# Performance work log

Measured on AMD Instinct MI355X. Metric: run time of the kernel, lower is better.

## Reference

```python
import jax, jax.numpy as jnp
import numpy as np

N, E, B = 50000, 800000, 64
H, D, FIN = 2, 128, 128  # heads, per-head dim, input feat dim
L = 2  # lstm layers


def segment_softmax(logits, seg, num_segments):
    # logits: [E, ...] softmax over entries sharing seg id (leading axis)
    m = jax.ops.segment_max(logits, seg, num_segments=num_segments)
    e = jnp.exp(logits - m[seg])
    s = jax.ops.segment_sum(e, seg, num_segments=num_segments)
    return e / s[seg]


def gat_layer(x, W, al, ar, b, src, dst):
    # DGL GATConv: fc -> per-edge LeakyReLU score -> edge softmax over dst -> aggregate
    h = (x @ W).reshape(N, H, D)                      # [N,H,D]
    el = jnp.sum(h * al, axis=-1)                     # [N,H]
    er = jnp.sum(h * ar, axis=-1)                     # [N,H]
    e = jax.nn.leaky_relu(el[src] + er[dst], 0.2)     # [E,H]
    alpha = segment_softmax(e, dst, N)                # [E,H]
    out = jax.ops.segment_sum(alpha[:, :, None] * h[src], dst, num_segments=N)
    return out + b                                    # [N,H,D]


def global_attention_pool(x, wg, bg, seg):
    gate = x @ wg + bg                                # [N,1]
    alpha = segment_softmax(gate, seg, B)             # [N,1]
    return jax.ops.segment_sum(alpha * x, seg, num_segments=B)  # [B,F]


def lstm(xs, Wih, Whh, bih, bhh):
    # xs: [T,B,Hd]; params stacked over layers [L,4Hd,Hd]/[L,4Hd]; torch gate order i,f,g,o
    Hd = Whh.shape[-1]
    h = None
    for l in range(Wih.shape[0]):
        def step(carry, x_t, l=l):
            h, c = carry
            gates = x_t @ Wih[l].T + h @ Whh[l].T + bih[l] + bhh[l]
            i, f, g, o = jnp.split(gates, 4, axis=-1)
            c = jax.nn.sigmoid(f) * c + jax.nn.sigmoid(i) * jnp.tanh(g)
            h = jax.nn.sigmoid(o) * jnp.tanh(c)
            return (h, c), h
        init = (jnp.zeros((xs.shape[1], Hd), xs.dtype), jnp.zeros((xs.shape[1], Hd), xs.dtype))
        (h, _), xs = jax.lax.scan(step, init, xs)
    return h  # final hidden state of last layer [B,Hd]


def setup_inputs() -> dict:
    key = jax.random.key(0)
    ks = jax.random.split(key, 32)
    s = 0.1
    inp = {
        "nfeats": jax.random.normal(ks[0], (N, FIN), jnp.float32),
        "src": jax.random.randint(ks[1], (E,), 0, N, jnp.int32),
        "dst": jax.random.randint(ks[2], (E,), 0, N, jnp.int32),
        "node_graph": jnp.sort(jax.random.randint(ks[3], (N,), 0, B, jnp.int32)),
    }
    for i, ink in enumerate([(FIN, ks[4], ks[5], ks[6], ks[7]), (D, ks[8], ks[9], ks[10], ks[11]), (D, ks[12], ks[13], ks[14], ks[15])]):
        fin, kw, kl, kr, kb = ink
        inp[f"W{i+1}"] = jax.random.normal(kw, (fin, H * D), jnp.float32) * s
        inp[f"al{i+1}"] = jax.random.normal(kl, (H, D), jnp.float32) * s
        inp[f"ar{i+1}"] = jax.random.normal(kr, (H, D), jnp.float32) * s
        inp[f"b{i+1}"] = jnp.zeros((H, D), jnp.float32)
    for i in range(4):
        inp[f"gw{i}"] = jax.random.normal(ks[16 + i], (D, 1), jnp.float32) * s
        inp[f"gb{i}"] = jnp.zeros((1,), jnp.float32)
    inp["Wih"] = jax.random.normal(ks[20], (L, 4 * D, D), jnp.float32) * s
    inp["Whh"] = jax.random.normal(ks[21], (L, 4 * D, D), jnp.float32) * s
    inp["bih"] = jnp.zeros((L, 4 * D), jnp.float32)
    inp["bhh"] = jnp.zeros((L, 4 * D), jnp.float32)
    inp["cw"] = jax.random.normal(ks[22], (D, 1), jnp.float32) * s
    inp["cb"] = jnp.zeros((1,), jnp.float32)
    return inp


def reference(nfeats, src, dst, node_graph,
              W1, al1, ar1, b1, W2, al2, ar2, b2, W3, al3, ar3, b3,
              gw0, gb0, gw1, gb1, gw2, gb2, gw3, gb3,
              Wih, Whh, bih, bhh, cw, cb):
    hg0 = global_attention_pool(nfeats, gw0, gb0, node_graph)
    h = jnp.mean(jax.nn.relu(gat_layer(nfeats, W1, al1, ar1, b1, src, dst)), axis=1)
    hg1 = global_attention_pool(h, gw1, gb1, node_graph)
    h = jnp.mean(jax.nn.relu(gat_layer(h, W2, al2, ar2, b2, src, dst)), axis=1)
    hg2 = global_attention_pool(h, gw2, gb2, node_graph)
    h = jnp.mean(jax.nn.relu(gat_layer(h, W3, al3, ar3, b3, src, dst)), axis=1)
    hg3 = global_attention_pool(h, gw3, gb3, node_graph)
    seq = jnp.stack((hg0, hg1, hg2, hg3), axis=0)     # [4,B,D]
    last_h = lstm(seq, Wih, Whh, bih, bhh)            # [B,D] (dropout: eval mode, identity)
    return jax.nn.sigmoid(last_h @ cw + cb)           # [B,1]
```

## Files before the change

### kernel.cpp

```cpp
#include <hip/hip_runtime.h>
#include <cmath>


typedef __attribute__((ext_vector_type(8))) short short8v;
typedef __attribute__((ext_vector_type(4))) float float4v;
typedef __attribute__((ext_vector_type(2))) float float2v;

__device__ __forceinline__ float sigmoidf_(float x){ return 1.f/(1.f+expf(-x)); }
__device__ __forceinline__ float fexp(float x){ return __expf(x); }

__device__ __forceinline__ unsigned f2bf_rne(float f){
  unsigned u = __float_as_uint(f);
  return (u + 0x7fffu + ((u >> 16) & 1u)) >> 16;
}
__device__ __forceinline__ float bf2f(ushort v){ return __uint_as_float((unsigned)v << 16); }
__device__ __forceinline__ unsigned char f2fp8(float f){
  unsigned v = __builtin_amdgcn_cvt_pk_fp8_f32(f, f, 0, false);
  return (unsigned char)(v & 0xffu);
}

__global__ void k_hist(const int* __restrict__ dst, int* __restrict__ deg, int E){
  int e = blockIdx.x*blockDim.x + threadIdx.x;
  if (e < E) atomicAdd(&deg[dst[e]], 1);
}

#define CHUNK 1024
__global__ __launch_bounds__(256) void k_chunksum(const int* __restrict__ in, int* __restrict__ csum, int n){
  int b = blockIdx.x;
  int tid = threadIdx.x;
  int v = 0;
  #pragma unroll
  for (int k = 0; k < 4; k++){
    int i = b*CHUNK + tid + k*256;
    if (i < n) v += in[i];
  }
  for (int d = 1; d < 64; d <<= 1) v += __shfl_xor(v, d);
  __shared__ int ws[4];
  if ((tid & 63) == 0) ws[tid>>6] = v;
  __syncthreads();
  if (tid == 0) csum[b] = ws[0]+ws[1]+ws[2]+ws[3];
}

__global__ void k_scan_small(const int* __restrict__ csum, int* __restrict__ cpre, int nb,
                             int* __restrict__ total_out){
  int lane = threadIdx.x;
  int v = (lane < nb) ? csum[lane] : 0;
  int incl = v;
  for (int d = 1; d < 64; d <<= 1){ int t = __shfl_up(incl, d); if (lane >= d) incl += t; }
  if (lane < nb) cpre[lane] = incl - v;
  if (lane == 63) *total_out = incl;
}

__global__ __launch_bounds__(256) void k_scan_apply(const int* __restrict__ in, const int* __restrict__ cpre,
                                                    int* __restrict__ offs, int n){
  int b = blockIdx.x;
  int tid = threadIdx.x, lane = tid & 63, wid = tid >> 6;
  int x[4];
  int s = 0;
  #pragma unroll
  for (int k = 0; k < 4; k++){
    int i = b*CHUNK + tid*4 + k;
    x[k] = (i < n) ? in[i] : 0;
    s += x[k];
  }
  int incl = s;
  for (int d = 1; d < 64; d <<= 1){ int t = __shfl_up(incl, d); if (lane >= d) incl += t; }
  __shared__ int ws[4];
  if (lane == 63) ws[wid] = incl;
  __syncthreads();
  int wpre = 0;
  for (int w = 0; w < wid; w++) wpre += ws[w];
  int base = cpre[b] + wpre + incl - s;
  #pragma unroll
  for (int k = 0; k < 4; k++){
    int i = b*CHUNK + tid*4 + k;
    if (i < n) offs[i] = base;
    base += x[k];
  }
}

__global__ void k_scatter_src(const int* __restrict__ src, const int* __restrict__ dst,
                              const int* __restrict__ offs, int* __restrict__ cnt,
                              int* __restrict__ srcP, int E){
  int e = blockIdx.x*blockDim.x + threadIdx.x;
  if (e < E){ int d = dst[e]; int p = atomicAdd(&cnt[d], 1); srcP[offs[d] + p] = src[e]; }
}

__global__ void k_graph_bounds(const int* __restrict__ ng, int* __restrict__ gstart, int n, int nb){
  int i = blockIdx.x*blockDim.x + threadIdx.x;
  if (i >= n) return;
  int g = ng[i];
  int gp = (i == 0) ? -1 : ng[i-1];
  for (int b = gp+1; b <= g; b++) gstart[b] = i;
  if (i == n-1) for (int b = g+1; b <= nb; b++) gstart[b] = n;
}

__global__ __launch_bounds__(256) void k_tobf16_gate(const float* __restrict__ in,
    const float* __restrict__ gw, const float* __restrict__ gb,
    ushort* __restrict__ out, float* __restrict__ gate, int Nn){
  int n = blockIdx.x*4 + (threadIdx.x >> 6);
  if (n >= Nn) return;
  int lane = threadIdx.x & 63;
  float2 v = *(const float2*)(in + (size_t)n*128 + lane*2);
  unsigned pk = (f2bf_rne(v.y) << 16) | f2bf_rne(v.x);
  *(unsigned*)(out + (size_t)n*128 + lane*2) = pk;
  float2 gv = *(const float2*)(gw + lane*2);
  float p = v.x*gv.x + v.y*gv.y;
  for (int k = 1; k < 64; k <<= 1) p += __shfl_xor(p, k);
  if (lane == 0) gate[n] = p + gb[0];
}

__global__ void k_wt(const float* __restrict__ W, ushort* __restrict__ Wt, int total){
  int idx = blockIdx.x*blockDim.x + threadIdx.x;
  if (idx >= total) return;
  int c = idx >> 7;
  int k = idx & 127;
  Wt[idx] = (ushort)f2bf_rne(W[(size_t)k*256 + c]);
}

__global__ void k_lstm_prep(const float* __restrict__ Wih, const float* __restrict__ Whh,
                            const float* __restrict__ bih, const float* __restrict__ bhh,
                            unsigned* __restrict__ Wxp, unsigned* __restrict__ Whp,
                            float* __restrict__ bias2){
  int idx = blockIdx.x*blockDim.x + threadIdx.x;
  if (idx >= 131072) return;
  int j   = idx & 511;
  int c   = (idx >> 9) & 63;
  int isH = (idx >> 15) & 1;
  int l   = idx >> 16;
  const float* srcW = isH ? Whh : Wih;
  float w0 = srcW[(size_t)l*512*128 + (size_t)j*128 + 2*c];
  float w1 = srcW[(size_t)l*512*128 + (size_t)j*128 + 2*c + 1];
  unsigned v = (f2bf_rne(w1) << 16) | f2bf_rne(w0);
  unsigned* dst = isH ? Whp : Wxp;
  dst[(size_t)l*32768 + c*512 + j] = v;
  if (!isH && c == 0) bias2[l*512 + j] = bih[l*512 + j] + bhh[l*512 + j];
}

__global__ __launch_bounds__(256) void k_gemm_mfma(const ushort* __restrict__ Xh,
    const ushort* __restrict__ Wt, const float* __restrict__ alv, const float* __restrict__ arv,
    unsigned char* __restrict__ Y8, float* __restrict__ el, float* __restrict__ er, int M){
  __shared__ ushort WlS[16*256*8];
  int tid = threadIdx.x;
  #pragma unroll
  for (int i = 0; i < 16; i++){
    int g = i*256 + tid;
    int row = g >> 4, c = g & 15;
    *(uint4*)(WlS + ((size_t)c*256 + row)*8) = *(const uint4*)(Wt + (size_t)row*128 + c*8);
  }
  __syncthreads();
  int wave = tid >> 6;
  int lane = tid & 63;
  int strip = blockIdx.x*4 + wave;
  if (strip*16 >= M) return;
  int m0 = strip*16;
  int l15 = lane & 15;
  int kg  = lane >> 4;
  int arow = m0 + l15; if (arow >= M) arow = M-1;
  short8v a[4];
  const ushort* xrow = Xh + (size_t)arow*128 + kg*8;
  #pragma unroll
  for (int ks = 0; ks < 4; ks++) a[ks] = *(const short8v*)(xrow + ks*32);
  float4v acc[16];
  #pragma unroll
  for (int nt = 0; nt < 16; nt++) acc[nt] = (float4v){0.f,0.f,0.f,0.f};
  #pragma unroll
  for (int nt = 0; nt < 16; nt++){
    #pragma unroll
    for (int ks = 0; ks < 4; ks++){
      short8v b = *(const short8v*)(WlS + (((size_t)(kg + ks*4)*256) + nt*16 + l15)*8);
      acc[nt] = __builtin_amdgcn_mfma_f32_16x16x32_bf16(a[ks], b, acc[nt], 0, 0, 0);
    }
  }
  float pel0[4]={0,0,0,0}, pel1[4]={0,0,0,0}, per0[4]={0,0,0,0}, per1[4]={0,0,0,0};
  #pragma unroll
  for (int nt = 0; nt < 16; nt++){
    int col = nt*16 + l15;
    float av = alv[col], rv = arv[col];
    #pragma unroll
    for (int j = 0; j < 4; j++){
      float v = acc[nt][j];
      int r = m0 + kg*4 + j;
      if (r < M) Y8[(size_t)r*256 + col] = f2fp8(v);
      if (nt < 8){ pel0[j] += v*av; per0[j] += v*rv; }
      else       { pel1[j] += v*av; per1[j] += v*rv; }
    }
  }
  #pragma unroll
  for (int j = 0; j < 4; j++){
    #pragma unroll
    for (int d = 1; d < 16; d <<= 1){
      pel0[j] += __shfl_xor(pel0[j], d);
      pel1[j] += __shfl_xor(pel1[j], d);
      per0[j] += __shfl_xor(per0[j], d);
      per1[j] += __shfl_xor(per1[j], d);
    }
  }
  if (l15 == 0){
    #pragma unroll
    for (int j = 0; j < 4; j++){
      int r = m0 + kg*4 + j;
      if (r < M){
        el[(size_t)r*2+0] = pel0[j];
        el[(size_t)r*2+1] = pel1[j];
        er[(size_t)r*2+0] = per0[j];
        er[(size_t)r*2+1] = per1[j];
      }
    }
  }
}

#define MAXE 256
__global__ __launch_bounds__(256) void k_aggregate(const unsigned char* __restrict__ hpair8,
    const float* __restrict__ el, const float* __restrict__ er,
    const int* __restrict__ srcP, const int* __restrict__ offs,
    const float* __restrict__ bias, const float* __restrict__ gwv, const float* __restrict__ gbv,
    ushort* __restrict__ outh, float* __restrict__ gate, int Nn){
  __shared__ float sw[4][MAXE][2];
  __shared__ int   ss[4][MAXE];
  int wave = threadIdx.x >> 6;
  int n = blockIdx.x*4 + wave;
  if (n >= Nn) return;
  int lane = threadIdx.x & 63;
  int e0 = offs[n], e1 = offs[n+1];
  int deg = e1 - e0;
  int quarter = lane >> 4;
  int sub     = lane & 15;
  int head    = sub >> 3;
  float2 erv = *(const float2*)(er + (size_t)n*2);
  float2v acc[8];
  #pragma unroll
  for (int k = 0; k < 8; k++) acc[k] = (float2v){0.f, 0.f};
  float inv0, inv1;

  if (deg <= MAXE){
    float m0 = -3.4e38f, m1 = -3.4e38f;
    for (int i = lane; i < deg; i += 64){
      int s = srcP[e0 + i];
      ss[wave][i] = s;
      float2 lv = *(const float2*)(el + (size_t)s*2);
      float v0 = lv.x + erv.x, v1 = lv.y + erv.y;
      v0 = (v0 > 0.f) ? v0 : 0.2f*v0;
      v1 = (v1 > 0.f) ? v1 : 0.2f*v1;
      sw[wave][i][0] = v0; sw[wave][i][1] = v1;
      m0 = fmaxf(m0, v0); m1 = fmaxf(m1, v1);
    }
    for (int k = 1; k < 64; k <<= 1){ m0 = fmaxf(m0, __shfl_xor(m0, k)); m1 = fmaxf(m1, __shfl_xor(m1, k)); }
    float s0 = 0.f, s1 = 0.f;
    for (int i = lane; i < deg; i += 64){
      float x0 = fexp(sw[wave][i][0] - m0);
      float x1 = fexp(sw[wave][i][1] - m1);
      sw[wave][i][0] = x0; sw[wave][i][1] = x1;
      s0 += x0; s1 += x1;
    }
    for (int k = 1; k < 64; k <<= 1){ s0 += __shfl_xor(s0, k); s1 += __shfl_xor(s1, k); }
    inv0 = (s0 > 0.f) ? 1.f/s0 : 0.f;
    inv1 = (s1 > 0.f) ? 1.f/s1 : 0.f;
    for (int i = quarter; i < deg; i += 4){
      int s = ss[wave][i];
      float w = sw[wave][i][head];
      uint4 hv = *(const uint4*)(hpair8 + (size_t)s*256 + sub*16);
      float2v wv = { w, w };
      acc[0] += wv*__builtin_amdgcn_cvt_pk_f32_fp8(hv.x, false);
      acc[1] += wv*__builtin_amdgcn_cvt_pk_f32_fp8(hv.x, true);
      acc[2] += wv*__builtin_amdgcn_cvt_pk_f32_fp8(hv.y, false);
      acc[3] += wv*__builtin_amdgcn_cvt_pk_f32_fp8(hv.y, true);
      acc[4] += wv*__builtin_amdgcn_cvt_pk_f32_fp8(hv.z, false);
      acc[5] += wv*__builtin_amdgcn_cvt_pk_f32_fp8(hv.z, true);
      acc[6] += wv*__builtin_amdgcn_cvt_pk_f32_fp8(hv.w, false);
      acc[7] += wv*__builtin_amdgcn_cvt_pk_f32_fp8(hv.w, true);
    }
  } else {
    float m0 = -3.4e38f, m1 = -3.4e38f;
    for (int i = e0 + lane; i < e1; i += 64){
      int s = srcP[i];
      float2 lv = *(const float2*)(el + (size_t)s*2);
      float v0 = lv.x + erv.x, v1 = lv.y + erv.y;
      v0 = (v0 > 0.f) ? v0 : 0.2f*v0;
      v1 = (v1 > 0.f) ? v1 : 0.2f*v1;
      m0 = fmaxf(m0, v0); m1 = fmaxf(m1, v1);
    }
    for (int k = 1; k < 64; k <<= 1){ m0 = fmaxf(m0, __shfl_xor(m0, k)); m1 = fmaxf(m1, __shfl_xor(m1, k)); }
    float s0 = 0.f, s1 = 0.f;
    for (int i = e0 + lane; i < e1; i += 64){
      int s = srcP[i];
      float2 lv = *(const float2*)(el + (size_t)s*2);
      float v0 = lv.x + erv.x, v1 = lv.y + erv.y;
      v0 = (v0 > 0.f) ? v0 : 0.2f*v0;
      v1 = (v1 > 0.f) ? v1 : 0.2f*v1;
      s0 += fexp(v0 - m0); s1 += fexp(v1 - m1);
    }
    for (int k = 1; k < 64; k <<= 1){ s0 += __shfl_xor(s0, k); s1 += __shfl_xor(s1, k); }
    inv0 = (s0 > 0.f) ? 1.f/s0 : 0.f;
    inv1 = (s1 > 0.f) ? 1.f/s1 : 0.f;
    for (int c0 = e0; c0 < e1; c0 += 64){
      int ce = e1 - c0; if (ce > 64) ce = 64;
      if (lane < ce){
        int s = srcP[c0 + lane];
        float2 lv = *(const float2*)(el + (size_t)s*2);
        float v0 = lv.x + erv.x, v1 = lv.y + erv.y;
        v0 = (v0 > 0.f) ? v0 : 0.2f*v0;
        v1 = (v1 > 0.f) ? v1 : 0.2f*v1;
        ss[wave][lane] = s;
        sw[wave][lane][0] = fexp(v0 - m0);
        sw[wave][lane][1] = fexp(v1 - m1);
      }
      for (int i = quarter; i < ce; i += 4){
        int s = ss[wave][i];
        float w = sw[wave][i][head];
        uint4 hv = *(const uint4*)(hpair8 + (size_t)s*256 + sub*16);
        float2v wv = { w, w };
        acc[0] += wv*__builtin_amdgcn_cvt_pk_f32_fp8(hv.x, false);
        acc[1] += wv*__builtin_amdgcn_cvt_pk_f32_fp8(hv.x, true);
        acc[2] += wv*__builtin_amdgcn_cvt_pk_f32_fp8(hv.y, false);
        acc[3] += wv*__builtin_amdgcn_cvt_pk_f32_fp8(hv.y, true);
        acc[4] += wv*__builtin_amdgcn_cvt_pk_f32_fp8(hv.z, false);
        acc[5] += wv*__builtin_amdgcn_cvt_pk_f32_fp8(hv.z, true);
        acc[6] += wv*__builtin_amdgcn_cvt_pk_f32_fp8(hv.w, false);
        acc[7] += wv*__builtin_amdgcn_cvt_pk_f32_fp8(hv.w, true);
      }
    }
  }

  float inv = head ? inv1 : inv0;
  #pragma unroll
  for (int k = 0; k < 8; k++){
    float2v t16, t32;
    t16[0] = __shfl_xor(acc[k][0], 16); t16[1] = __shfl_xor(acc[k][1], 16);
    acc[k] += t16;
    t32[0] = __shfl_xor(acc[k][0], 32); t32[1] = __shfl_xor(acc[k][1], 32);
    acc[k] += t32;
  }
  float t[16];
  #pragma unroll
  for (int k = 0; k < 16; k++)
    t[k] = fmaxf(acc[k>>1][k&1]*inv + bias[sub*16 + k], 0.f);
  float o[16];
  #pragma unroll
  for (int k = 0; k < 16; k++) o[k] = 0.5f*(t[k] + __shfl_xor(t[k], 8));
  if (lane < 8){
    ushort u[16];
    #pragma unroll
    for (int k = 0; k < 16; k++) u[k] = (ushort)f2bf_rne(o[k]);
    *(uint4*)(outh + (size_t)n*128 + sub*16)     = *(uint4*)u;
    *(uint4*)(outh + (size_t)n*128 + sub*16 + 8) = *(uint4*)(u + 8);
    float gp = 0.f;
    #pragma unroll
    for (int k = 0; k < 16; k++) gp += o[k]*gwv[sub*16 + k];
    #pragma unroll
    for (int d = 1; d < 8; d <<= 1) gp += __shfl_xor(gp, d);
    if (sub == 0) gate[n] = gp + gbv[0];
  }
}

#define POOL_P 32
__global__ __launch_bounds__(128) void k_pool_partial(const ushort* __restrict__ x,
    const float* __restrict__ gate, const int* __restrict__ gstart,
    float* __restrict__ partials){
  int b = blockIdx.x;
  int p = blockIdx.y;
  int n0 = gstart[b], n1 = gstart[b+1];
  int tid = threadIdx.x, lane = tid & 63, wid = tid >> 6;
  __shared__ float red[2];
  float m = -3.4e38f;
  for (int n = n0 + tid; n < n1; n += 128) m = fmaxf(m, gate[n]);
  for (int k = 1; k < 64; k <<= 1) m = fmaxf(m, __shfl_xor(m, k));
  if (lane == 0) red[wid] = m;
  __syncthreads();
  m = fmaxf(red[0], red[1]);
  __syncthreads();
  float s = 0.f;
  for (int n = n0 + tid; n < n1; n += 128) s += __expf(gate[n] - m);
  for (int k = 1; k < 64; k <<= 1) s += __shfl_xor(s, k);
  if (lane == 0) red[wid] = s;
  __syncthreads();
  s = red[0] + red[1];
  float inv = (s > 0.f) ? 1.f/s : 0.f;
  float acc = 0.f;
  for (int n = n0 + p; n < n1; n += POOL_P){
    float w = __expf(gate[n] - m) * inv;
    acc += w * bf2f(x[(size_t)n*128 + tid]);
  }
  partials[((size_t)b*POOL_P + p)*128 + tid] = acc;
}

__global__ __launch_bounds__(128) void k_pool_reduce(const float* __restrict__ partials,
    float* __restrict__ hg){
  int b = blockIdx.x;
  int tid = threadIdx.x;
  float s = 0.f;
  #pragma unroll
  for (int p = 0; p < POOL_P; p++) s += partials[((size_t)b*POOL_P + p)*128 + tid];
  hg[(size_t)b*128 + tid] = s;
}

__global__ __launch_bounds__(512) void k_lstm_all(const float* __restrict__ seq,
    const unsigned* __restrict__ Wxp, const unsigned* __restrict__ Whp,
    const float* __restrict__ bias2,
    const float* __restrict__ cw, const float* __restrict__ cb,
    float* __restrict__ out, int B){
  int b = blockIdx.x;
  int j = threadIdx.x;
  __shared__ float xs[4][128];
  __shared__ float gates[512];
  __shared__ float hcur[128], ccur[128];
  __shared__ float l0out[4][128];
  __shared__ float red[2];

  #pragma unroll
  for (int l = 0; l < 2; l++){
    const unsigned* Wx = Wxp + (size_t)l*32768;
    const unsigned* Wh = Whp + (size_t)l*32768;
    const float* bi = bias2 + l*512;
    { int t = j >> 7, k = j & 127;
      xs[t][k] = (l == 0) ? seq[(size_t)t*B*128 + (size_t)b*128 + k] : l0out[t][k];
      if (j < 128){ hcur[j] = 0.f; ccur[j] = 0.f; } }
    __syncthreads();
    float gx[4] = {0.f, 0.f, 0.f, 0.f};
    #pragma unroll 8
    for (int c = 0; c < 64; c++){
      unsigned w2 = Wx[c*512 + j];
      float wlo = __uint_as_float(w2 << 16);
      float whi = __uint_as_float(w2 & 0xffff0000u);
      #pragma unroll
      for (int t = 0; t < 4; t++)
        gx[t] += xs[t][2*c]*wlo + xs[t][2*c+1]*whi;
    }
    #pragma unroll
    for (int t = 0; t < 4; t++){
      float g = gx[t] + bi[j];
      #pragma unroll 8
      for (int c = 0; c < 64; c++){
        unsigned w2 = Wh[c*512 + j];
        g += hcur[2*c]*__uint_as_float(w2 << 16)
           + hcur[2*c+1]*__uint_as_float(w2 & 0xffff0000u);
      }
      gates[j] = g;
      __syncthreads();
      if (j < 128){
        float gi = sigmoidf_(gates[j]);
        float gf = sigmoidf_(gates[128 + j]);
        float gg = tanhf(gates[256 + j]);
        float go = sigmoidf_(gates[384 + j]);
        float c2 = gf * ccur[j] + gi * gg;
        float h = go * tanhf(c2);
        ccur[j] = c2;
        hcur[j] = h;
        if (l == 0) l0out[t][j] = h;
      }
      __syncthreads();
    }
  }
  float p = (j < 128) ? hcur[j] * cw[j] : 0.f;
  if (j < 128){
    for (int k = 1; k < 64; k <<= 1) p += __shfl_xor(p, k);
    if ((j & 63) == 0) red[j >> 6] = p;
  }
  __syncthreads();
  if (j == 0) out[b] = sigmoidf_(red[0] + red[1] + cb[0]);
}

extern "C" void kernel_launch(void* const* d_in, const int* in_sizes, int n_in,
                              void* d_out, int out_size, void* d_ws, size_t ws_size,
                              hipStream_t stream){
  const float* nfeats = (const float*)d_in[0];
  const int*   src    = (const int*)d_in[1];
  const int*   dst    = (const int*)d_in[2];
  const int*   ng     = (const int*)d_in[3];
  const float* Wm[3]  = { (const float*)d_in[4],  (const float*)d_in[8],  (const float*)d_in[12] };
  const float* al[3]  = { (const float*)d_in[5],  (const float*)d_in[9],  (const float*)d_in[13] };
  const float* ar[3]  = { (const float*)d_in[6],  (const float*)d_in[10], (const float*)d_in[14] };
  const float* bb[3]  = { (const float*)d_in[7],  (const float*)d_in[11], (const float*)d_in[15] };
  const float* gw[4]  = { (const float*)d_in[16], (const float*)d_in[18], (const float*)d_in[20], (const float*)d_in[22] };
  const float* gb[4]  = { (const float*)d_in[17], (const float*)d_in[19], (const float*)d_in[21], (const float*)d_in[23] };
  const float* Wih = (const float*)d_in[24];
  const float* Whh = (const float*)d_in[25];
  const float* bih = (const float*)d_in[26];
  const float* bhh = (const float*)d_in[27];
  const float* cw  = (const float*)d_in[28];
  const float* cb  = (const float*)d_in[29];

  const int N = in_sizes[3];
  const int E = in_sizes[1];
  const int B = out_size;

  char* p = (char*)d_ws;
  auto alloc = [&](size_t bytes) -> void* {
    void* q = (void*)p;
    p += (bytes + 255) & ~(size_t)255;
    return q;
  };
  unsigned char* hpair8 = (unsigned char*)alloc((size_t)N*256);
  ushort* aggh   = (ushort*)alloc((size_t)N*128*2);
  ushort* xh0    = (ushort*)alloc((size_t)N*128*2);
  ushort* Wt     = (ushort*)alloc((size_t)3*256*128*2);
  float*  el     = (float*)alloc((size_t)N*2*4);
  float*  er     = (float*)alloc((size_t)N*2*4);
  int*    srcP   = (int*)alloc((size_t)E*4);
  float*  gate   = (float*)alloc((size_t)N*4);
  int*    deg    = (int*)alloc((size_t)N*4);
  int*    offs   = (int*)alloc((size_t)(N+1)*4);
  int*    cnt    = (int*)alloc((size_t)N*4);
  int*    gstart = (int*)alloc((size_t)(B+1)*4);
  int*    csum   = (int*)alloc((size_t)64*4);
  int*    cpre   = (int*)alloc((size_t)64*4);
  float*  seqA   = (float*)alloc((size_t)4*B*128*4);
  float*  partials = (float*)alloc((size_t)B*POOL_P*128*4);
  unsigned* Wxp  = (unsigned*)alloc((size_t)2*64*512*4);
  unsigned* Whp  = (unsigned*)alloc((size_t)2*64*512*4);
  float*  bias2  = (float*)alloc((size_t)2*512*4);

  auto cdiv = [](int a, int b){ return (a + b - 1) / b; };
  const int NB = cdiv(N, CHUNK);

  hipMemsetAsync(deg, 0, (size_t)N*4, stream);
  hipMemsetAsync(cnt, 0, (size_t)N*4, stream);
  k_hist<<<cdiv(E,256), 256, 0, stream>>>(dst, deg, E);
  k_chunksum<<<NB, 256, 0, stream>>>(deg, csum, N);
  k_scan_small<<<1, 64, 0, stream>>>(csum, cpre, NB, offs + N);
  k_scan_apply<<<NB, 256, 0, stream>>>(deg, cpre, offs, N);
  k_scatter_src<<<cdiv(E,256), 256, 0, stream>>>(src, dst, offs, cnt, srcP, E);
  k_graph_bounds<<<cdiv(N,256), 256, 0, stream>>>(ng, gstart, N, B);

  k_tobf16_gate<<<cdiv(N,4), 256, 0, stream>>>(nfeats, gw[0], gb[0], xh0, gate, N);
  for (int l = 0; l < 3; l++)
    k_wt<<<cdiv(256*128, 256), 256, 0, stream>>>(Wm[l], Wt + (size_t)l*256*128, 256*128);
  k_lstm_prep<<<cdiv(131072, 256), 256, 0, stream>>>(Wih, Whh, bih, bhh, Wxp, Whp, bias2);

  auto pool_rest = [&](const ushort* xv, float* hgv){
    dim3 pg(B, POOL_P);
    k_pool_partial<<<pg, 128, 0, stream>>>(xv, gate, gstart, partials);
    k_pool_reduce<<<B, 128, 0, stream>>>(partials, hgv);
  };

  pool_rest(xh0, seqA + 0*(size_t)B*128);

  const ushort* xh = xh0;
  const int strips = cdiv(N, 16);
  for (int layer = 0; layer < 3; layer++){
    k_gemm_mfma<<<cdiv(strips,4), 256, 0, stream>>>(xh, Wt + (size_t)layer*256*128,
        al[layer], ar[layer], hpair8, el, er, N);
    k_aggregate<<<cdiv(N,4), 256, 0, stream>>>(hpair8, el, er, srcP, offs,
        bb[layer], gw[layer+1], gb[layer+1], aggh, gate, N);
    pool_rest(aggh, seqA + (size_t)(layer+1)*B*128);
    xh = aggh;
  }

  k_lstm_all<<<B, 512, 0, stream>>>(seqA, Wxp, Whp, bias2, cw, cb, (float*)d_out, B);
}
```

Before: 422.8 us.

## Fuse prep kernels, co-schedule pooling with GEMM, fold scan and pool reduction

```diff
diff --git a/kernel.cpp b/kernel.cpp
--- a/kernel.cpp
+++ b/kernel.cpp
@@ -41,20 +41,19 @@
   if (tid == 0) csum[b] = ws[0]+ws[1]+ws[2]+ws[3];
 }
 
-__global__ void k_scan_small(const int* __restrict__ csum, int* __restrict__ cpre, int nb,
-                             int* __restrict__ total_out){
-  int lane = threadIdx.x;
-  int v = (lane < nb) ? csum[lane] : 0;
-  int incl = v;
-  for (int d = 1; d < 64; d <<= 1){ int t = __shfl_up(incl, d); if (lane >= d) incl += t; }
-  if (lane < nb) cpre[lane] = incl - v;
-  if (lane == 63) *total_out = incl;
-}
-
-__global__ __launch_bounds__(256) void k_scan_apply(const int* __restrict__ in, const int* __restrict__ cpre,
-                                                    int* __restrict__ offs, int n){
+__global__ __launch_bounds__(256) void k_scan_apply(const int* __restrict__ in, const int* __restrict__ csum,
+                                                    int* __restrict__ offs, int n, int nb){
   int b = blockIdx.x;
   int tid = threadIdx.x, lane = tid & 63, wid = tid >> 6;
+  __shared__ int s_cpre;
+  __shared__ int ws[4];
+  if (tid < 64){
+    int v = (tid < nb) ? csum[tid] : 0;
+    int icl = v;
+    for (int d = 1; d < 64; d <<= 1){ int t = __shfl_up(icl, d); if (lane >= d) icl += t; }
+    if (tid == b) s_cpre = icl - v;
+  }
+  __syncthreads();
   int x[4];
   int s = 0;
   #pragma unroll
@@ -65,18 +64,18 @@
   }
   int incl = s;
   for (int d = 1; d < 64; d <<= 1){ int t = __shfl_up(incl, d); if (lane >= d) incl += t; }
-  __shared__ int ws[4];
   if (lane == 63) ws[wid] = incl;
   __syncthreads();
   int wpre = 0;
   for (int w = 0; w < wid; w++) wpre += ws[w];
-  int base = cpre[b] + wpre + incl - s;
+  int base = s_cpre + wpre + incl - s;
   #pragma unroll
   for (int k = 0; k < 4; k++){
     int i = b*CHUNK + tid*4 + k;
     if (i < n) offs[i] = base;
     base += x[k];
   }
+  if (b == nb-1 && tid == 255) offs[n] = base;
 }
 
 __global__ void k_scatter_src(const int* __restrict__ src, const int* __restrict__ dst,
@@ -86,127 +85,176 @@
   if (e < E){ int d = dst[e]; int p = atomicAdd(&cnt[d], 1); srcP[offs[d] + p] = src[e]; }
 }
 
-__global__ void k_graph_bounds(const int* __restrict__ ng, int* __restrict__ gstart, int n, int nb){
-  int i = blockIdx.x*blockDim.x + threadIdx.x;
-  if (i >= n) return;
-  int g = ng[i];
-  int gp = (i == 0) ? -1 : ng[i-1];
-  for (int b = gp+1; b <= g; b++) gstart[b] = i;
-  if (i == n-1) for (int b = g+1; b <= nb; b++) gstart[b] = n;
-}
-
-__global__ __launch_bounds__(256) void k_tobf16_gate(const float* __restrict__ in,
-    const float* __restrict__ gw, const float* __restrict__ gb,
-    ushort* __restrict__ out, float* __restrict__ gate, int Nn){
-  int n = blockIdx.x*4 + (threadIdx.x >> 6);
-  if (n >= Nn) return;
-  int lane = threadIdx.x & 63;
-  float2 v = *(const float2*)(in + (size_t)n*128 + lane*2);
-  unsigned pk = (f2bf_rne(v.y) << 16) | f2bf_rne(v.x);
-  *(unsigned*)(out + (size_t)n*128 + lane*2) = pk;
-  float2 gv = *(const float2*)(gw + lane*2);
-  float p = v.x*gv.x + v.y*gv.y;
-  for (int k = 1; k < 64; k <<= 1) p += __shfl_xor(p, k);
-  if (lane == 0) gate[n] = p + gb[0];
-}
-
-__global__ void k_wt(const float* __restrict__ W, ushort* __restrict__ Wt, int total){
-  int idx = blockIdx.x*blockDim.x + threadIdx.x;
-  if (idx >= total) return;
-  int c = idx >> 7;
-  int k = idx & 127;
-  Wt[idx] = (ushort)f2bf_rne(W[(size_t)k*256 + c]);
-}
-
-__global__ void k_lstm_prep(const float* __restrict__ Wih, const float* __restrict__ Whh,
-                            const float* __restrict__ bih, const float* __restrict__ bhh,
-                            unsigned* __restrict__ Wxp, unsigned* __restrict__ Whp,
-                            float* __restrict__ bias2){
-  int idx = blockIdx.x*blockDim.x + threadIdx.x;
-  if (idx >= 131072) return;
-  int j   = idx & 511;
-  int c   = (idx >> 9) & 63;
-  int isH = (idx >> 15) & 1;
-  int l   = idx >> 16;
-  const float* srcW = isH ? Whh : Wih;
-  float w0 = srcW[(size_t)l*512*128 + (size_t)j*128 + 2*c];
-  float w1 = srcW[(size_t)l*512*128 + (size_t)j*128 + 2*c + 1];
-  unsigned v = (f2bf_rne(w1) << 16) | f2bf_rne(w0);
-  unsigned* dst = isH ? Whp : Wxp;
-  dst[(size_t)l*32768 + c*512 + j] = v;
-  if (!isH && c == 0) bias2[l*512 + j] = bih[l*512 + j] + bhh[l*512 + j];
-}
-
-__global__ __launch_bounds__(256) void k_gemm_mfma(const ushort* __restrict__ Xh,
+__global__ __launch_bounds__(256) void k_prep(
+    const int* __restrict__ ng, int* __restrict__ gstart,
+    const float* __restrict__ nfeats, const float* __restrict__ gw0, const float* __restrict__ gb0,
+    ushort* __restrict__ xh0, float* __restrict__ gate,
+    const float* __restrict__ W0, const float* __restrict__ W1, const float* __restrict__ W2,
+    ushort* __restrict__ Wt,
+    const float* __restrict__ Wih, const float* __restrict__ Whh,
+    const float* __restrict__ bih, const float* __restrict__ bhh,
+    unsigned* __restrict__ Wxp, unsigned* __restrict__ Whp, float* __restrict__ bias2,
+    int N, int B){
+  int tid = threadIdx.x;
+  int blk = blockIdx.x;
+  const int nbGB = (N + 255) >> 8;
+  const int nbTG = (N + 3) >> 2;
+  const int nbWT = (3*256*128) >> 8;
+  if (blk < nbGB){
+    int i = blk*256 + tid;
+    if (i >= N) return;
+    int g = ng[i];
+    int gp = (i == 0) ? -1 : ng[i-1];
+    for (int bb = gp+1; bb <= g; bb++) gstart[bb] = i;
+    if (i == N-1) for (int bb = g+1; bb <= B; bb++) gstart[bb] = N;
+    return;
+  }
+  blk -= nbGB;
+  if (blk < nbTG){
+    int n = blk*4 + (tid >> 6);
+    if (n >= N) return;
+    int lane = tid & 63;
+    float2 v = *(const float2*)(nfeats + (size_t)n*128 + lane*2);
+    unsigned pk = (f2bf_rne(v.y) << 16) | f2bf_rne(v.x);
+    *(unsigned*)(xh0 + (size_t)n*128 + lane*2) = pk;
+    float2 gv = *(const float2*)(gw0 + lane*2);
+    float p = v.x*gv.x + v.y*gv.y;
+    for (int k = 1; k < 64; k <<= 1) p += __shfl_xor(p, k);
+    if (lane == 0) gate[n] = p + gb0[0];
+    return;
+  }
+  blk -= nbTG;
+  if (blk < nbWT){
+    int idx = blk*256 + tid;
+    int layer = idx >> 15;
+    int within = idx & 32767;
+    int c = within >> 7;
+    int k = within & 127;
+    const float* W = (layer == 0) ? W0 : (layer == 1) ? W1 : W2;
+    Wt[idx] = (ushort)f2bf_rne(W[(size_t)k*256 + c]);
+    return;
+  }
+  blk -= nbWT;
+  {
+    int idx = blk*256 + tid;
+    if (idx >= 131072) return;
+    int j   = idx & 511;
+    int c   = (idx >> 9) & 63;
+    int isH = (idx >> 15) & 1;
+    int l   = idx >> 16;
+    const float* srcW = isH ? Whh : Wih;
+    float w0 = srcW[(size_t)l*512*128 + (size_t)j*128 + 2*c];
+    float w1 = srcW[(size_t)l*512*128 + (size_t)j*128 + 2*c + 1];
+    unsigned v = (f2bf_rne(w1) << 16) | f2bf_rne(w0);
+    unsigned* dstp = isH ? Whp : Wxp;
+    dstp[(size_t)l*32768 + c*512 + j] = v;
+    if (!isH && c == 0) bias2[l*512 + j] = bih[l*512 + j] + bhh[l*512 + j];
+  }
+}
+
+__global__ __launch_bounds__(256) void k_gemm_pool(const ushort* __restrict__ Xh,
     const ushort* __restrict__ Wt, const float* __restrict__ alv, const float* __restrict__ arv,
-    unsigned char* __restrict__ Y8, float* __restrict__ el, float* __restrict__ er, int M){
+    unsigned char* __restrict__ Y8, float* __restrict__ el, float* __restrict__ er, int M,
+    int gemmBlocks, const float* __restrict__ gate, const int* __restrict__ gstart,
+    float* __restrict__ partials){
   __shared__ ushort WlS[16*256*8];
   int tid = threadIdx.x;
-  #pragma unroll
-  for (int i = 0; i < 16; i++){
-    int g = i*256 + tid;
-    int row = g >> 4, c = g & 15;
-    *(uint4*)(WlS + ((size_t)c*256 + row)*8) = *(const uint4*)(Wt + (size_t)row*128 + c*8);
-  }
-  __syncthreads();
-  int wave = tid >> 6;
-  int lane = tid & 63;
-  int strip = blockIdx.x*4 + wave;
-  if (strip*16 >= M) return;
-  int m0 = strip*16;
-  int l15 = lane & 15;
-  int kg  = lane >> 4;
-  int arow = m0 + l15; if (arow >= M) arow = M-1;
-  short8v a[4];
-  const ushort* xrow = Xh + (size_t)arow*128 + kg*8;
-  #pragma unroll
-  for (int ks = 0; ks < 4; ks++) a[ks] = *(const short8v*)(xrow + ks*32);
-  float4v acc[16];
-  #pragma unroll
-  for (int nt = 0; nt < 16; nt++) acc[nt] = (float4v){0.f,0.f,0.f,0.f};
-  #pragma unroll
-  for (int nt = 0; nt < 16; nt++){
-    #pragma unroll
-    for (int ks = 0; ks < 4; ks++){
-      short8v b = *(const short8v*)(WlS + (((size_t)(kg + ks*4)*256) + nt*16 + l15)*8);
-      acc[nt] = __builtin_amdgcn_mfma_f32_16x16x32_bf16(a[ks], b, acc[nt], 0, 0, 0);
-    }
-  }
-  float pel0[4]={0,0,0,0}, pel1[4]={0,0,0,0}, per0[4]={0,0,0,0}, per1[4]={0,0,0,0};
-  #pragma unroll
-  for (int nt = 0; nt < 16; nt++){
-    int col = nt*16 + l15;
-    float av = alv[col], rv = arv[col];
+  if ((int)blockIdx.x < gemmBlocks){
+    #pragma unroll
+    for (int i = 0; i < 16; i++){
+      int g = i*256 + tid;
+      int row = g >> 4, c = g & 15;
+      *(uint4*)(WlS + ((size_t)c*256 + row)*8) = *(const uint4*)(Wt + (size_t)row*128 + c*8);
+    }
+    __syncthreads();
+    int wave = tid >> 6;
+    int lane = tid & 63;
+    int strip = blockIdx.x*4 + wave;
+    if (strip*16 >= M) return;
+    int m0 = strip*16;
+    int l15 = lane & 15;
+    int kg  = lane >> 4;
+    int arow = m0 + l15; if (arow >= M) arow = M-1;
+    short8v a[4];
+    const ushort* xrow = Xh + (size_t)arow*128 + kg*8;
+    #pragma unroll
+    for (int ks = 0; ks < 4; ks++) a[ks] = *(const short8v*)(xrow + ks*32);
+    float4v acc[16];
+    #pragma unroll
+    for (int nt = 0; nt < 16; nt++) acc[nt] = (float4v){0.f,0.f,0.f,0.f};
+    #pragma unroll
+    for (int nt = 0; nt < 16; nt++){
+      #pragma unroll
+      for (int ks = 0; ks < 4; ks++){
+        short8v b = *(const short8v*)(WlS + (((size_t)(kg + ks*4)*256) + nt*16 + l15)*8);
+        acc[nt] = __builtin_amdgcn_mfma_f32_16x16x32_bf16(a[ks], b, acc[nt], 0, 0, 0);
+      }
+    }
+    float pel0[4]={0,0,0,0}, pel1[4]={0,0,0,0}, per0[4]={0,0,0,0}, per1[4]={0,0,0,0};
+    #pragma unroll
+    for (int nt = 0; nt < 16; nt++){
+      int col = nt*16 + l15;
+      float av = alv[col], rv = arv[col];
+      #pragma unroll
+      for (int j = 0; j < 4; j++){
+        float v = acc[nt][j];
+        int r = m0 + kg*4 + j;
+        if (r < M) Y8[(size_t)r*256 + col] = f2fp8(v);
+        if (nt < 8){ pel0[j] += v*av; per0[j] += v*rv; }
+        else       { pel1[j] += v*av; per1[j] += v*rv; }
+      }
+    }
     #pragma unroll
     for (int j = 0; j < 4; j++){
-      float v = acc[nt][j];
-      int r = m0 + kg*4 + j;
-      if (r < M) Y8[(size_t)r*256 + col] = f2fp8(v);
-      if (nt < 8){ pel0[j] += v*av; per0[j] += v*rv; }
-      else       { pel1[j] += v*av; per1[j] += v*rv; }
-    }
-  }
-  #pragma unroll
-  for (int j = 0; j < 4; j++){
-    #pragma unroll
-    for (int d = 1; d < 16; d <<= 1){
-      pel0[j] += __shfl_xor(pel0[j], d);
-      pel1[j] += __shfl_xor(pel1[j], d);
-      per0[j] += __shfl_xor(per0[j], d);
-      per1[j] += __shfl_xor(per1[j], d);
-    }
-  }
-  if (l15 == 0){
-    #pragma unroll
-    for (int j = 0; j < 4; j++){
-      int r = m0 + kg*4 + j;
-      if (r < M){
-        el[(size_t)r*2+0] = pel0[j];
-        el[(size_t)r*2+1] = pel1[j];
-        er[(size_t)r*2+0] = per0[j];
-        er[(size_t)r*2+1] = per1[j];
-      }
-    }
+      #pragma unroll
+      for (int d = 1; d < 16; d <<= 1){
+        pel0[j] += __shfl_xor(pel0[j], d);
+        pel1[j] += __shfl_xor(pel1[j], d);
+        per0[j] += __shfl_xor(per0[j], d);
+        per1[j] += __shfl_xor(per1[j], d);
+      }
+    }
+    if (l15 == 0){
+      #pragma unroll
+      for (int j = 0; j < 4; j++){
+        int r = m0 + kg*4 + j;
+        if (r < M){
+          el[(size_t)r*2+0] = pel0[j];
+          el[(size_t)r*2+1] = pel1[j];
+          er[(size_t)r*2+0] = per0[j];
+          er[(size_t)r*2+1] = per1[j];
+        }
+      }
+    }
+  } else {
+    float* red = (float*)WlS;
+    int pb = blockIdx.x - gemmBlocks;
+    int b = pb >> 4;
+    int py = pb & 15;
+    int lane = tid & 63, wid = tid >> 6;
+    int n0 = gstart[b], n1 = gstart[b+1];
+    float m = -3.4e38f;
+    for (int n = n0 + tid; n < n1; n += 256) m = fmaxf(m, gate[n]);
+    for (int k = 1; k < 64; k <<= 1) m = fmaxf(m, __shfl_xor(m, k));
+    if (lane == 0) red[wid] = m;
+    __syncthreads();
+    m = fmaxf(fmaxf(red[0], red[1]), fmaxf(red[2], red[3]));
+    __syncthreads();
+    float s = 0.f;
+    for (int n = n0 + tid; n < n1; n += 256) s += __expf(gate[n] - m);
+    for (int k = 1; k < 64; k <<= 1) s += __shfl_xor(s, k);
+    if (lane == 0) red[wid] = s;
+    __syncthreads();
+    s = red[0] + red[1] + red[2] + red[3];
+    float inv = (s > 0.f) ? 1.f/s : 0.f;
+    int half = tid >> 7, t127 = tid & 127;
+    int p = py*2 + half;
+    float acc = 0.f;
+    for (int n = n0 + p; n < n1; n += 32){
+      float w = __expf(gate[n] - m) * inv;
+      acc += w * bf2f(Xh[(size_t)n*128 + t127]);
+    }
+    partials[((size_t)b*32 + p)*128 + t127] = acc;
   }
 }
 
@@ -353,48 +401,7 @@
   }
 }
 
-#define POOL_P 32
-__global__ __launch_bounds__(128) void k_pool_partial(const ushort* __restrict__ x,
-    const float* __restrict__ gate, const int* __restrict__ gstart,
-    float* __restrict__ partials){
-  int b = blockIdx.x;
-  int p = blockIdx.y;
-  int n0 = gstart[b], n1 = gstart[b+1];
-  int tid = threadIdx.x, lane = tid & 63, wid = tid >> 6;
-  __shared__ float red[2];
-  float m = -3.4e38f;
-  for (int n = n0 + tid; n < n1; n += 128) m = fmaxf(m, gate[n]);
-  for (int k = 1; k < 64; k <<= 1) m = fmaxf(m, __shfl_xor(m, k));
-  if (lane == 0) red[wid] = m;
-  __syncthreads();
-  m = fmaxf(red[0], red[1]);
-  __syncthreads();
-  float s = 0.f;
-  for (int n = n0 + tid; n < n1; n += 128) s += __expf(gate[n] - m);
-  for (int k = 1; k < 64; k <<= 1) s += __shfl_xor(s, k);
-  if (lane == 0) red[wid] = s;
-  __syncthreads();
-  s = red[0] + red[1];
-  float inv = (s > 0.f) ? 1.f/s : 0.f;
-  float acc = 0.f;
-  for (int n = n0 + p; n < n1; n += POOL_P){
-    float w = __expf(gate[n] - m) * inv;
-    acc += w * bf2f(x[(size_t)n*128 + tid]);
-  }
-  partials[((size_t)b*POOL_P + p)*128 + tid] = acc;
-}
-
-__global__ __launch_bounds__(128) void k_pool_reduce(const float* __restrict__ partials,
-    float* __restrict__ hg){
-  int b = blockIdx.x;
-  int tid = threadIdx.x;
-  float s = 0.f;
-  #pragma unroll
-  for (int p = 0; p < POOL_P; p++) s += partials[((size_t)b*POOL_P + p)*128 + tid];
-  hg[(size_t)b*128 + tid] = s;
-}
-
-__global__ __launch_bounds__(512) void k_lstm_all(const float* __restrict__ seq,
+__global__ __launch_bounds__(512) void k_lstm_all(const float* __restrict__ part4,
     const unsigned* __restrict__ Wxp, const unsigned* __restrict__ Whp,
     const float* __restrict__ bias2,
     const float* __restrict__ cw, const float* __restrict__ cb,
@@ -413,7 +420,15 @@
     const unsigned* Wh = Whp + (size_t)l*32768;
     const float* bi = bias2 + l*512;
     { int t = j >> 7, k = j & 127;
-      xs[t][k] = (l == 0) ? seq[(size_t)t*B*128 + (size_t)b*128 + k] : l0out[t][k];
+      if (l == 0){
+        const float* pp = part4 + (((size_t)t*B + b)*32)*128 + k;
+        float s = 0.f;
+        #pragma unroll
+        for (int p2 = 0; p2 < 32; p2++) s += pp[p2*128];
+        xs[t][k] = s;
+      } else {
+        xs[t][k] = l0out[t][k];
+      }
       if (j < 128){ hcur[j] = 0.f; ccur[j] = 0.f; } }
     __syncthreads();
     float gx[4] = {0.f, 0.f, 0.f, 0.f};
@@ -499,13 +514,11 @@
   int*    srcP   = (int*)alloc((size_t)E*4);
   float*  gate   = (float*)alloc((size_t)N*4);
   int*    deg    = (int*)alloc((size_t)N*4);
+  int*    cnt    = (int*)alloc((size_t)N*4);
   int*    offs   = (int*)alloc((size_t)(N+1)*4);
-  int*    cnt    = (int*)alloc((size_t)N*4);
   int*    gstart = (int*)alloc((size_t)(B+1)*4);
   int*    csum   = (int*)alloc((size_t)64*4);
-  int*    cpre   = (int*)alloc((size_t)64*4);
-  float*  seqA   = (float*)alloc((size_t)4*B*128*4);
-  float*  partials = (float*)alloc((size_t)B*POOL_P*128*4);
+  float*  part4  = (float*)alloc((size_t)4*B*32*128*4);
   unsigned* Wxp  = (unsigned*)alloc((size_t)2*64*512*4);
   unsigned* Whp  = (unsigned*)alloc((size_t)2*64*512*4);
   float*  bias2  = (float*)alloc((size_t)2*512*4);
@@ -513,38 +526,34 @@
   auto cdiv = [](int a, int b){ return (a + b - 1) / b; };
   const int NB = cdiv(N, CHUNK);
 
-  hipMemsetAsync(deg, 0, (size_t)N*4, stream);
-  hipMemsetAsync(cnt, 0, (size_t)N*4, stream);
+  hipMemsetAsync(deg, 0, (size_t)((char*)cnt - (char*)deg) + (size_t)N*4, stream);
   k_hist<<<cdiv(E,256), 256, 0, stream>>>(dst, deg, E);
   k_chunksum<<<NB, 256, 0, stream>>>(deg, csum, N);
-  k_scan_small<<<1, 64, 0, stream>>>(csum, cpre, NB, offs + N);
-  k_scan_apply<<<NB, 256, 0, stream>>>(deg, cpre, offs, N);
+  k_scan_apply<<<NB, 256, 0, stream>>>(deg, csum, offs, N, NB);
   k_scatter_src<<<cdiv(E,256), 256, 0, stream>>>(src, dst, offs, cnt, srcP, E);
-  k_graph_bounds<<<cdiv(N,256), 256, 0, stream>>>(ng, gstart, N, B);
-
-  k_tobf16_gate<<<cdiv(N,4), 256, 0, stream>>>(nfeats, gw[0], gb[0], xh0, gate, N);
-  for (int l = 0; l < 3; l++)
-    k_wt<<<cdiv(256*128, 256), 256, 0, stream>>>(Wm[l], Wt + (size_t)l*256*128, 256*128);
-  k_lstm_prep<<<cdiv(131072, 256), 256, 0, stream>>>(Wih, Whh, bih, bhh, Wxp, Whp, bias2);
-
-  auto pool_rest = [&](const ushort* xv, float* hgv){
-    dim3 pg(B, POOL_P);
-    k_pool_partial<<<pg, 128, 0, stream>>>(xv, gate, gstart, partials);
-    k_pool_reduce<<<B, 128, 0, stream>>>(partials, hgv);
-  };
-
-  pool_rest(xh0, seqA + 0*(size_t)B*128);
+
+  {
+    int nbGB = cdiv(N,256), nbTG = cdiv(N,4), nbWT = (3*256*128)/256, nbLP = cdiv(131072,256);
+    k_prep<<<nbGB + nbTG + nbWT + nbLP, 256, 0, stream>>>(
+        ng, gstart, nfeats, gw[0], gb[0], xh0, gate,
+        Wm[0], Wm[1], Wm[2], Wt, Wih, Whh, bih, bhh, Wxp, Whp, bias2, N, B);
+  }
+
+  const int strips = cdiv(N, 16);
+  const int gemmBlocks = cdiv(strips, 4);
+  const int poolBlocks = B*16;
 
   const ushort* xh = xh0;
-  const int strips = cdiv(N, 16);
   for (int layer = 0; layer < 3; layer++){
-    k_gemm_mfma<<<cdiv(strips,4), 256, 0, stream>>>(xh, Wt + (size_t)layer*256*128,
-        al[layer], ar[layer], hpair8, el, er, N);
+    k_gemm_pool<<<gemmBlocks + poolBlocks, 256, 0, stream>>>(xh, Wt + (size_t)layer*256*128,
+        al[layer], ar[layer], hpair8, el, er, N, gemmBlocks, gate, gstart,
+        part4 + (size_t)layer*B*32*128);
     k_aggregate<<<cdiv(N,4), 256, 0, stream>>>(hpair8, el, er, srcP, offs,
         bb[layer], gw[layer+1], gb[layer+1], aggh, gate, N);
-    pool_rest(aggh, seqA + (size_t)(layer+1)*B*128);
     xh = aggh;
   }
-
-  k_lstm_all<<<B, 512, 0, stream>>>(seqA, Wxp, Whp, bias2, cw, cb, (float*)d_out, B);
-}
+  k_gemm_pool<<<poolBlocks, 256, 0, stream>>>(aggh, Wt, al[0], ar[0], hpair8, el, er, N,
+      0, gate, gstart, part4 + (size_t)3*B*32*128);
+
+  k_lstm_all<<<B, 512, 0, stream>>>(part4, Wxp, Whp, bias2, cw, cb, (float*)d_out, B);
+}
```

Result: slower. 433.3 us (+2.5%).
